# Kernel tuning notes

Measured on AMD Instinct MI355X. Metric: run time of the kernel, lower is better.

The kernel has to match this reference:

```python
import jax, jax.numpy as jnp
import numpy as np

B, S, D = 2, 2048, 1024
H, DK, DV = 16, 64, 64
D_OUT = 1024


def setup_inputs() -> dict:
    key = jax.random.key(0)
    ks = jax.random.split(key, 9)
    sd = 1.0 / np.sqrt(D)
    # Linear weights stored as [in, out] (torch applies x @ W.T with W [out,in])
    return {
        "x": jax.random.normal(ks[0], (B, S, D), dtype=jnp.float32),
        "Wq": jax.random.normal(ks[1], (D, H * DK), dtype=jnp.float32) * sd,
        "bq": jnp.zeros((H * DK,), dtype=jnp.float32),
        "Wk": jax.random.normal(ks[2], (D, H * DK), dtype=jnp.float32) * sd,
        "bk": jnp.zeros((H * DK,), dtype=jnp.float32),
        "Wv": jax.random.normal(ks[3], (D, H * DV), dtype=jnp.float32) * sd,
        "bv": jnp.zeros((H * DV,), dtype=jnp.float32),
        "Wo": jax.random.normal(ks[4], (H * DV, D_OUT), dtype=jnp.float32) * sd,
        "bo": jnp.zeros((D_OUT,), dtype=jnp.float32),
    }


def _attn(x, Wq, bq, Wk, bk, Wv, bv, Wo, bo):
    n = x.shape[-2]
    q = (x @ Wq + bq).reshape(B, n, H, DK).transpose(0, 2, 1, 3)  # [B,H,S,DK]
    k = (x @ Wk + bk).reshape(B, n, H, DK).transpose(0, 2, 1, 3)
    v = (x @ Wv + bv).reshape(B, n, H, DV).transpose(0, 2, 1, 3)
    scores = jnp.einsum("bhqd,bhkd->bhqk", q / jnp.sqrt(jnp.float32(DK)), k)
    # causal additive mask: 0 on/below diagonal, -inf above (matches 1 - 1/tril)
    causal = jnp.tril(jnp.ones((n, n), dtype=bool))
    scores = jnp.where(causal, scores, -jnp.inf)
    probs = jax.nn.softmax(scores, axis=-1)
    out = jnp.einsum("bhqk,bhkd->bhqd", probs, v)  # [B,H,S,DV]
    out = out.transpose(0, 2, 1, 3).reshape(B, n, H * DV)
    return out @ Wo + bo


def reference(x, Wq, bq, Wk, bk, Wv, bv, Wo, bo):
    return _attn(x, Wq, bq, Wk, bk, Wv, bv, Wo, bo)
```

## Files before the change

### kernel.cpp

```cpp
#include <hip/hip_runtime.h>

typedef unsigned short u16;
typedef __bf16 bf16_t;
typedef bf16_t bf16x8 __attribute__((ext_vector_type(8)));
typedef float f32x4 __attribute__((ext_vector_type(4)));

#define DEV __device__ __forceinline__
#define LOG2E 1.4426950408889634f
#define QKS (0.125f * LOG2E)

static_assert(sizeof(bf16x8) == 16, "bf16x8 must be 16B");

DEV u16 f2b(float v) { return __builtin_bit_cast(u16, (bf16_t)v); }
DEV float b2f(u16 v) { return (float)__builtin_bit_cast(bf16_t, v); }

DEV void g2l16(const void* g, void* l) {
  __builtin_amdgcn_global_load_lds(
      (const __attribute__((address_space(1))) void*)g,
      (__attribute__((address_space(3))) void*)l, 16, 0, 0);
}

DEV int sniff_is_f32(const u16* __restrict__ W) {
  const int lane = threadIdx.x & 63;
  int cnt = 0;
#pragma unroll
  for (int i = 0; i < 8; i++) {
    u16 u = W[(lane * 8 + i) * 2];
    cnt += (((u >> 7) & 0xFF) >= 126) ? 1 : 0;
  }
#pragma unroll
  for (int off = 1; off < 64; off <<= 1) cnt += __shfl_xor(cnt, off, 64);
  return cnt > 128;
}


__global__ __launch_bounds__(256) void convert_x_k(
    const void* __restrict__ xin, const u16* __restrict__ Wsniff,
    u16* __restrict__ xb) {
  const int i = (blockIdx.x * 256 + threadIdx.x) * 8;
  if (sniff_is_f32(Wsniff)) {
    const float* xf = (const float*)xin;
    float4 a = *(const float4*)&xf[i];
    float4 b = *(const float4*)&xf[i + 4];
    u16 o[8] = {f2b(a.x), f2b(a.y), f2b(a.z), f2b(a.w),
                f2b(b.x), f2b(b.y), f2b(b.z), f2b(b.w)};
    *(uint4*)&xb[i] = *(const uint4*)o;
  } else {
    *(uint4*)&xb[i] = *(const uint4*)((const u16*)xin + i);
  }
}

__global__ __launch_bounds__(256) void transpose_k(
    const void* __restrict__ Wq, const void* __restrict__ Wk,
    const void* __restrict__ Wv, const void* __restrict__ Wo,
    const void* __restrict__ bq, const void* __restrict__ bk,
    const void* __restrict__ bv, const void* __restrict__ bo,
    u16* __restrict__ Wqkv_t, u16* __restrict__ Wo_t,
    u16* __restrict__ bqkv_b, u16* __restrict__ bo_b) {
  __shared__ u16 tile[64][68];
  const int z = blockIdx.z;
  const void* src = (z == 0) ? Wq : (z == 1) ? Wk : (z == 2) ? Wv : Wo;
  u16* dst = (z < 3) ? (Wqkv_t + (size_t)z * 1024 * 1024) : Wo_t;
  const int k0 = blockIdx.y * 64, n0 = blockIdx.x * 64;
  const int t = threadIdx.x;
  const int r = t >> 4, c4 = (t & 15) * 4;
  const int isf = sniff_is_f32((const u16*)Wq);

  if (blockIdx.x == 0 && blockIdx.y == 0) {
    const void* bsrc = (z == 0) ? bq : (z == 1) ? bk : (z == 2) ? bv : bo;
    u16* bdst = (z < 3) ? (bqkv_b + z * 1024) : bo_b;
#pragma unroll
    for (int i = 0; i < 4; i++) {
      const int idx = t + i * 256;
      const float v =
          isf ? ((const float*)bsrc)[idx] : b2f(((const u16*)bsrc)[idx]);
      bdst[idx] = f2b(v);
    }
  }

#pragma unroll
  for (int i = 0; i < 4; i++) {
    int rr = r + i * 16;
    const size_t base = (size_t)(k0 + rr) * 1024 + n0 + c4;
    if (isf) {
      float4 v = *(const float4*)((const float*)src + base);
      tile[rr][c4] = f2b(v.x); tile[rr][c4 + 1] = f2b(v.y);
      tile[rr][c4 + 2] = f2b(v.z); tile[rr][c4 + 3] = f2b(v.w);
    } else {
      ushort4 v = *(const ushort4*)((const u16*)src + base);
      tile[rr][c4] = v.x; tile[rr][c4 + 1] = v.y;
      tile[rr][c4 + 2] = v.z; tile[rr][c4 + 3] = v.w;
    }
  }
  __syncthreads();
#pragma unroll
  for (int i = 0; i < 4; i++) {
    int rr = r + i * 16;
    ushort4 v;
    v.x = tile[c4][rr]; v.y = tile[c4 + 1][rr];
    v.z = tile[c4 + 2][rr]; v.w = tile[c4 + 3][rr];
    *(ushort4*)&dst[(size_t)(n0 + rr) * 1024 + k0 + c4] = v;
  }
}

template <int MODE>
__global__ __launch_bounds__(256, 3) void gemm_k(
    const u16* __restrict__ A, const u16* __restrict__ Bt,
    const u16* __restrict__ bias, void* __restrict__ o0v,
    u16* __restrict__ o1, u16* __restrict__ o2,
    const u16* __restrict__ Wsniff, int M, int N, int K) {
  alignas(16) __shared__ u16 smem[2][128][64];
  u16(*As)[64] = smem[0];
  u16(*Bs)[64] = smem[1];
  const int tid = threadIdx.x;
  const int wave = tid >> 6, lane = tid & 63;
  const int quad = lane >> 4, l16 = lane & 15;
  const int m0 = blockIdx.y * 128, n0 = blockIdx.x * 128;
  const int wr = (wave >> 1) * 64, wc = (wave & 1) * 64;
  const int sw = l16 & 7;

  f32x4 acc[4][4];
#pragma unroll
  for (int i = 0; i < 4; i++)
#pragma unroll
    for (int j = 0; j < 4; j++) acc[i][j] = (f32x4){0.f, 0.f, 0.f, 0.f};

  const int srow = lane >> 3, schunk = lane & 7;
  const int cs = schunk ^ srow;

  for (int k0 = 0; k0 < K; k0 += 64) {
    __syncthreads();
#pragma unroll
    for (int j = 0; j < 8; j++) {
      const int t = wave * 8 + j;
      if (t < 16) {
        const int row = t * 8 + srow;
        g2l16(&A[(size_t)(m0 + row) * K + k0 + cs * 8], &As[t * 8][0]);
      } else {
        const int t2 = t - 16;
        const int row = t2 * 8 + srow;
        g2l16(&Bt[(size_t)(n0 + row) * K + k0 + cs * 8], &Bs[t2 * 8][0]);
      }
    }
    __syncthreads();
#pragma unroll
    for (int kk = 0; kk < 2; kk++) {
      const int pos = ((kk << 2) | quad) ^ sw;
      bf16x8 af[4], bfr[4];
#pragma unroll
      for (int mi = 0; mi < 4; mi++)
        af[mi] = *(const bf16x8*)&As[wr + mi * 16 + l16][pos * 8];
#pragma unroll
      for (int ni = 0; ni < 4; ni++)
        bfr[ni] = *(const bf16x8*)&Bs[wc + ni * 16 + l16][pos * 8];
#pragma unroll
      for (int mi = 0; mi < 4; mi++)
#pragma unroll
        for (int ni = 0; ni < 4; ni++)
          acc[mi][ni] = __builtin_amdgcn_mfma_f32_16x16x32_bf16(
              af[mi], bfr[ni], acc[mi][ni], 0, 0, 0);
    }
  }

  if (MODE == 0 && n0 >= 2048) {
    u16* T = &smem[0][0][0];
    const int b = m0 >> 11, sb = m0 & 2047;
#pragma unroll
    for (int r2 = 0; r2 < 2; r2++) {
      __syncthreads();
      if (wc == r2 * 64) {
#pragma unroll
        for (int mi = 0; mi < 4; mi++)
#pragma unroll
          for (int ni = 0; ni < 4; ni++) {
            const int c = ni * 16 + l16;
            const int col = n0 + r2 * 64 + c;
            const float bv_ = b2f(bias[col]);
#pragma unroll
            for (int r = 0; r < 4; r++) {
              const int s = wr + mi * 16 + quad * 4 + r;
              T[c * 136 + s] = f2b(acc[mi][ni][r] + bv_);
            }
          }
      }
      __syncthreads();
      {
        const int c = tid >> 2, s8 = (tid & 3) * 32;
        const int nn = (n0 - 2048) + r2 * 64 + c;
        const int h = nn >> 6, d = nn & 63;
        u16* dst = &o2[(((size_t)(b * 16 + h) * 64) + d) * 2048 + sb];
#pragma unroll
        for (int j2 = 0; j2 < 4; j2++)
          *(uint4*)&dst[s8 + j2 * 8] = *(const uint4*)&T[c * 136 + s8 + j2 * 8];
      }
    }
    return;
  }

  const int isf = (MODE == 1) ? sniff_is_f32(Wsniff) : 0;
#pragma unroll
  for (int mi = 0; mi < 4; mi++) {
    const int rbase = m0 + wr + mi * 16 + quad * 4;
#pragma unroll
    for (int ni = 0; ni < 4; ni++) {
      const int col = n0 + wc + ni * 16 + l16;
      const float bv_ = b2f(bias[col]);
      if (MODE == 0) {
        const int seg = col >> 10;
        const int nn = col & 1023;
        const int h = nn >> 6, d = nn & 63;
        u16* op = (seg == 0) ? (u16*)o0v : o1;
#pragma unroll
        for (int r = 0; r < 4; r++) {
          const int m = rbase + r;
          const int b = m >> 11, s = m & 2047;
          float v = acc[mi][ni][r] + bv_;
          if (seg == 0) v *= QKS;
          op[(((size_t)(b * 16 + h) * 2048) + s) * 64 + d] = f2b(v);
        }
      } else {
#pragma unroll
        for (int r = 0; r < 4; r++) {
          const int m = rbase + r;
          const float v = acc[mi][ni][r] + bv_;
          if (isf) ((float*)o0v)[(size_t)m * N + col] = v;
          else     ((u16*)o0v)[(size_t)m * N + col] = f2b(v);
        }
      }
    }
  }
}

__global__ __launch_bounds__(512, 4) void attn_k(
    const u16* __restrict__ Q, const u16* __restrict__ K,
    const u16* __restrict__ Vt, u16* __restrict__ p0, u16* __restrict__ p1,
    float* __restrict__ l0, float* __restrict__ l1) {
  alignas(16) __shared__ u16 Ks[2][128][64];
  alignas(16) __shared__ u16 Vs[2][64][128];
  alignas(16) __shared__ u16 PsT[128][64];
  const int tid = threadIdx.x;
  const int w = tid >> 6, lane = tid & 63;
  const int quad = lane >> 4, l16 = lane & 15;
  const int split = blockIdx.x & 1;
  const int pairIdx = blockIdx.x >> 1;
  const int bh = blockIdx.y;
  const int b = bh >> 4, h = bh & 15;
  const int sw = l16 & 7;

  u16* Op = split ? p1 : p0;
  float* lp = split ? l1 : l0;

  const int krow_off = lane >> 3, kchunk = lane & 7;
  const int vrow_off = lane >> 4, vchunk = lane & 15;

  for (int pi = 0; pi < 2; pi++) {
    const int qt = pi ? (15 - pairIdx) : pairIdx;
    const int q0 = qt * 128;
    const int wrow = q0 + w * 16;
    const int nkt = qt + 1;
    const int cnt = (nkt - split + 1) >> 1;

    bf16x8 aq[2];
#pragma unroll
    for (int kc = 0; kc < 2; kc++)
      aq[kc] = *(const bf16x8*)&Q[((size_t)bh * 2048 + wrow + l16) * 64 +
                                  kc * 32 + quad * 8];

    f32x4 oacc[4];
#pragma unroll
    for (int di = 0; di < 4; di++) oacc[di] = (f32x4){0.f, 0.f, 0.f, 0.f};
    float lrp = 0.f;

    auto stage = [&](int buf, int kts) {
      const int k0s = kts * 128;
#pragma unroll
      for (int j = 0; j < 4; j++) {
        const int t = w * 4 + j;
        if (t < 16) {
          const int r = t * 8 + krow_off;
          const int cs = kchunk ^ (r & 7);
          g2l16(&K[((size_t)bh * 2048 + k0s + r) * 64 + cs * 8],
                &Ks[buf][t * 8][0]);
        } else {
          const int t2 = t - 16;
          const int r = t2 * 4 + vrow_off;
          const int cs = vchunk ^ (r & 7);
          g2l16(&Vt[((size_t)bh * 64 + r) * 2048 + k0s + cs * 8],
                &Vs[buf][t2 * 4][0]);
        }
      }
    };

    if (cnt > 0) stage(0, split);
    for (int ti = 0; ti < cnt; ti++) {
      const int cur = ti & 1;
      const int k0 = (split + 2 * ti) * 128;
      if (ti + 1 < cnt) {
        stage(cur ^ 1, split + 2 * (ti + 1));
        asm volatile("s_waitcnt vmcnt(4)" ::: "memory");
      } else {
        asm volatile("s_waitcnt vmcnt(0)" ::: "memory");
      }
      asm volatile("s_barrier" ::: "memory");

#pragma unroll
      for (int h2 = 0; h2 < 2; h2++) {
        const int k0h = k0 + h2 * 64;
        if (k0h > wrow + 15) continue;
        const bool needmask = (k0h + 63 > wrow);

        f32x4 st[4];
#pragma unroll
        for (int nk = 0; nk < 4; nk++) st[nk] = (f32x4){0.f, 0.f, 0.f, 0.f};
#pragma unroll
        for (int kc = 0; kc < 2; kc++)
#pragma unroll
          for (int nk = 0; nk < 4; nk++) {
            const int pos = ((kc << 2) | quad) ^ sw;
            bf16x8 kf =
                *(const bf16x8*)&Ks[cur][h2 * 64 + nk * 16 + l16][pos * 8];
            st[nk] = __builtin_amdgcn_mfma_f32_16x16x32_bf16(kf, aq[kc],
                                                             st[nk], 0, 0, 0);
          }

        const int q_glob = wrow + l16;
#pragma unroll
        for (int nk = 0; nk < 4; nk++) {
          const int kbase = k0h + nk * 16 + quad * 4;
          u16 pk[4];
#pragma unroll
          for (int r = 0; r < 4; r++) {
            float p = __builtin_amdgcn_exp2f(st[nk][r]);
            if (needmask && (kbase + r > q_glob)) p = 0.f;
            lrp += p;
            pk[r] = f2b(p);
          }
          const int g = nk * 4 + quad;
          const int cc = (g >> 1) ^ sw;
          *(uint2*)&PsT[w * 16 + l16][cc * 8 + (g & 1) * 4] =
              *(const uint2*)pk;
        }
        asm volatile("s_waitcnt lgkmcnt(0)" ::: "memory");

#pragma unroll
        for (int kc = 0; kc < 2; kc++) {
          const int pcc = ((kc << 2) | quad) ^ sw;
          bf16x8 ap = *(const bf16x8*)&PsT[w * 16 + l16][pcc * 8];
#pragma unroll
          for (int di = 0; di < 4; di++) {
            const int pos = ((h2 << 3) | (kc << 2) | quad) ^ sw;
            bf16x8 vf = *(const bf16x8*)&Vs[cur][di * 16 + l16][pos * 8];
            oacc[di] = __builtin_amdgcn_mfma_f32_16x16x32_bf16(
                ap, vf, oacc[di], 0, 0, 0);
          }
        }
      }
      asm volatile("s_barrier" ::: "memory");
    }

    lrp += __shfl_xor(lrp, 16, 64);
    lrp += __shfl_xor(lrp, 32, 64);
    if (lane < 16) lp[(size_t)bh * 2048 + wrow + lane] = lrp;

#pragma unroll
    for (int di = 0; di < 4; di++)
#pragma unroll
      for (int r = 0; r < 4; r++) {
        const int row = wrow + quad * 4 + r;
        Op[((size_t)b * 2048 + row) * 1024 + h * 64 + di * 16 + l16] =
            f2b(oacc[di][r]);
      }
  }
}

__global__ __launch_bounds__(256) void norm_k(
    const u16* __restrict__ p0, const u16* __restrict__ p1,
    const float* __restrict__ l0, const float* __restrict__ l1,
    u16* __restrict__ out) {
  const int i = (blockIdx.x * 256 + threadIdx.x) * 8;
  const int row = i >> 10;
  const int col = i & 1023;
  const int bh = ((row >> 11) << 4) | (col >> 6);
  const int q = row & 2047;
  const size_t li = (size_t)bh * 2048 + q;
  const float rc = 1.0f / (l0[li] + l1[li]);
  uint4 a = *(const uint4*)&p0[i];
  uint4 bb = *(const uint4*)&p1[i];
  const u16* au = (const u16*)&a;
  const u16* bu = (const u16*)&bb;
  u16 o[8];
#pragma unroll
  for (int j = 0; j < 8; j++) o[j] = f2b((b2f(au[j]) + b2f(bu[j])) * rc);
  *(uint4*)&out[i] = *(const uint4*)o;
}

extern "C" void kernel_launch(void* const* d_in, const int* in_sizes, int n_in,
                              void* d_out, int out_size, void* d_ws,
                              size_t ws_size, hipStream_t stream) {
  const void* x  = d_in[0];
  const void* Wq = d_in[1];
  const void* bq = d_in[2];
  const void* Wk = d_in[3];
  const void* bk = d_in[4];
  const void* Wv = d_in[5];
  const void* bv = d_in[6];
  const void* Wo = d_in[7];
  const void* bo = d_in[8];

  char* ws = (char*)d_ws;
  u16* xb     = (u16*)ws;          ws += (size_t)4096 * 1024 * 2;
  u16* Wqkv_t = (u16*)ws;          ws += (size_t)3072 * 1024 * 2;
  u16* Wo_t   = (u16*)ws;          ws += (size_t)1024 * 1024 * 2;
  u16* bqkv_b = (u16*)ws;          ws += 3072 * 2;
  u16* bo_b   = (u16*)ws;          ws += 1024 * 2 + 128;
  u16* Qb     = (u16*)ws;          ws += (size_t)4096 * 1024 * 2;
  u16* Kb     = (u16*)ws;          ws += (size_t)4096 * 1024 * 2;
  u16* Vtb    = (u16*)ws;          ws += (size_t)4096 * 1024 * 2;
  u16* p1     = (u16*)ws;          ws += (size_t)4096 * 1024 * 2;
  float* l0   = (float*)ws;        ws += (size_t)32 * 2048 * 4;
  float* l1   = (float*)ws;        ws += (size_t)32 * 2048 * 4;
  u16* p0     = xb;
  u16* Ob     = xb;

  convert_x_k<<<2048, 256, 0, stream>>>(x, (const u16*)Wq, xb);
  transpose_k<<<dim3(16, 16, 4), 256, 0, stream>>>(Wq, Wk, Wv, Wo, bq, bk, bv,
                                                   bo, Wqkv_t, Wo_t, bqkv_b,
                                                   bo_b);
  gemm_k<0><<<dim3(24, 32), 256, 0, stream>>>(xb, Wqkv_t, bqkv_b, Qb, Kb, Vtb,
                                              (const u16*)Wq, 4096, 3072, 1024);
  attn_k<<<dim3(16, 32), 512, 0, stream>>>(Qb, Kb, Vtb, p0, p1, l0, l1);
  norm_k<<<2048, 256, 0, stream>>>(p0, p1, l0, l1, Ob);
  gemm_k<1><<<dim3(8, 32), 256, 0, stream>>>(Ob, Wo_t, bo_b, d_out, nullptr,
                                             nullptr, (const u16*)Wq, 4096,
                                             1024, 1024);
}
```

Before: 199.2 us.

## Merge x conversion into weight prep kernel and pipeline both attention query tiles

Folds the x fp32-to-bf16 conversion into the weight transpose kernel as an extra grid slice, removing one kernel launch. In the attention kernel, the two query tiles each block handles are processed in one continuous K/V tile loop instead of two separate loops. This lets the double-buffered prefetch of the second tile's first K/V block overlap the first tile's last compute, so the pipeline no longer drains and refills between tiles. It keeps Q fragments for both tiles in registers, which raises register pressure, and adds a mid-loop epilogue plus accumulator reset.

```diff
diff --git a/kernel.cpp b/kernel.cpp
--- a/kernel.cpp
+++ b/kernel.cpp
@@ -34,37 +34,43 @@
 }
 
 
-__global__ __launch_bounds__(256) void convert_x_k(
-    const void* __restrict__ xin, const u16* __restrict__ Wsniff,
-    u16* __restrict__ xb) {
-  const int i = (blockIdx.x * 256 + threadIdx.x) * 8;
-  if (sniff_is_f32(Wsniff)) {
-    const float* xf = (const float*)xin;
-    float4 a = *(const float4*)&xf[i];
-    float4 b = *(const float4*)&xf[i + 4];
-    u16 o[8] = {f2b(a.x), f2b(a.y), f2b(a.z), f2b(a.w),
-                f2b(b.x), f2b(b.y), f2b(b.z), f2b(b.w)};
-    *(uint4*)&xb[i] = *(const uint4*)o;
-  } else {
-    *(uint4*)&xb[i] = *(const uint4*)((const u16*)xin + i);
-  }
-}
-
-__global__ __launch_bounds__(256) void transpose_k(
+__global__ __launch_bounds__(256) void prep_k(
     const void* __restrict__ Wq, const void* __restrict__ Wk,
     const void* __restrict__ Wv, const void* __restrict__ Wo,
     const void* __restrict__ bq, const void* __restrict__ bk,
     const void* __restrict__ bv, const void* __restrict__ bo,
-    u16* __restrict__ Wqkv_t, u16* __restrict__ Wo_t,
-    u16* __restrict__ bqkv_b, u16* __restrict__ bo_b) {
+    const void* __restrict__ xin, u16* __restrict__ Wqkv_t,
+    u16* __restrict__ Wo_t, u16* __restrict__ bqkv_b, u16* __restrict__ bo_b,
+    u16* __restrict__ xb) {
   __shared__ u16 tile[64][68];
   const int z = blockIdx.z;
+  const int t = threadIdx.x;
+  const int isf = sniff_is_f32((const u16*)Wq);
+
+  if (z == 4) {
+    const int bi = blockIdx.y * 16 + blockIdx.x;
+    const int base = bi * 16384 + t * 8;
+#pragma unroll
+    for (int it = 0; it < 8; it++) {
+      const int i = base + it * 2048;
+      if (isf) {
+        const float* xf = (const float*)xin;
+        float4 a = *(const float4*)&xf[i];
+        float4 b = *(const float4*)&xf[i + 4];
+        u16 o[8] = {f2b(a.x), f2b(a.y), f2b(a.z), f2b(a.w),
+                    f2b(b.x), f2b(b.y), f2b(b.z), f2b(b.w)};
+        *(uint4*)&xb[i] = *(const uint4*)o;
+      } else {
+        *(uint4*)&xb[i] = *(const uint4*)((const u16*)xin + i);
+      }
+    }
+    return;
+  }
+
   const void* src = (z == 0) ? Wq : (z == 1) ? Wk : (z == 2) ? Wv : Wo;
   u16* dst = (z < 3) ? (Wqkv_t + (size_t)z * 1024 * 1024) : Wo_t;
   const int k0 = blockIdx.y * 64, n0 = blockIdx.x * 64;
-  const int t = threadIdx.x;
   const int r = t >> 4, c4 = (t & 15) * 4;
-  const int isf = sniff_is_f32((const u16*)Wq);
 
   if (blockIdx.x == 0 && blockIdx.y == 0) {
     const void* bsrc = (z == 0) ? bq : (z == 1) ? bk : (z == 2) ? bv : bo;
@@ -253,115 +259,55 @@
   const int krow_off = lane >> 3, kchunk = lane & 7;
   const int vrow_off = lane >> 4, vchunk = lane & 15;
 
-  for (int pi = 0; pi < 2; pi++) {
-    const int qt = pi ? (15 - pairIdx) : pairIdx;
-    const int q0 = qt * 128;
-    const int wrow = q0 + w * 16;
-    const int nkt = qt + 1;
-    const int cnt = (nkt - split + 1) >> 1;
-
-    bf16x8 aq[2];
+  const int qtA = pairIdx, qtB = 15 - pairIdx;
+  const int cntA = (qtA + 2 - split) >> 1;
+  const int cntB = (qtB + 2 - split) >> 1;
+  const int tot = cntA + cntB;
+  const int wrowP[2] = {qtA * 128 + w * 16, qtB * 128 + w * 16};
+
+  bf16x8 aq[2][2];
+#pragma unroll
+  for (int pi = 0; pi < 2; pi++)
 #pragma unroll
     for (int kc = 0; kc < 2; kc++)
-      aq[kc] = *(const bf16x8*)&Q[((size_t)bh * 2048 + wrow + l16) * 64 +
-                                  kc * 32 + quad * 8];
-
-    f32x4 oacc[4];
-#pragma unroll
-    for (int di = 0; di < 4; di++) oacc[di] = (f32x4){0.f, 0.f, 0.f, 0.f};
-    float lrp = 0.f;
-
-    auto stage = [&](int buf, int kts) {
-      const int k0s = kts * 128;
-#pragma unroll
-      for (int j = 0; j < 4; j++) {
-        const int t = w * 4 + j;
-        if (t < 16) {
-          const int r = t * 8 + krow_off;
-          const int cs = kchunk ^ (r & 7);
-          g2l16(&K[((size_t)bh * 2048 + k0s + r) * 64 + cs * 8],
-                &Ks[buf][t * 8][0]);
-        } else {
-          const int t2 = t - 16;
-          const int r = t2 * 4 + vrow_off;
-          const int cs = vchunk ^ (r & 7);
-          g2l16(&Vt[((size_t)bh * 64 + r) * 2048 + k0s + cs * 8],
-                &Vs[buf][t2 * 4][0]);
-        }
-      }
-    };
-
-    if (cnt > 0) stage(0, split);
-    for (int ti = 0; ti < cnt; ti++) {
-      const int cur = ti & 1;
-      const int k0 = (split + 2 * ti) * 128;
-      if (ti + 1 < cnt) {
-        stage(cur ^ 1, split + 2 * (ti + 1));
-        asm volatile("s_waitcnt vmcnt(4)" ::: "memory");
+      aq[pi][kc] = *(const bf16x8*)&Q[((size_t)bh * 2048 + wrowP[pi] + l16) *
+                                          64 + kc * 32 + quad * 8];
+
+  f32x4 oacc[4];
+#pragma unroll
+  for (int di = 0; di < 4; di++) oacc[di] = (f32x4){0.f, 0.f, 0.f, 0.f};
+  float lrp = 0.f;
+
+  auto tileK0 = [&](int idx) {
+    const int ti = (idx >= cntA) ? idx - cntA : idx;
+    return (split + 2 * ti) * 128;
+  };
+
+  auto stage = [&](int buf, int k0s) {
+#pragma unroll
+    for (int j = 0; j < 4; j++) {
+      const int t = w * 4 + j;
+      if (t < 16) {
+        const int r = t * 8 + krow_off;
+        const int cs = kchunk ^ (r & 7);
+        g2l16(&K[((size_t)bh * 2048 + k0s + r) * 64 + cs * 8],
+              &Ks[buf][t * 8][0]);
       } else {
-        asm volatile("s_waitcnt vmcnt(0)" ::: "memory");
-      }
-      asm volatile("s_barrier" ::: "memory");
-
-#pragma unroll
-      for (int h2 = 0; h2 < 2; h2++) {
-        const int k0h = k0 + h2 * 64;
-        if (k0h > wrow + 15) continue;
-        const bool needmask = (k0h + 63 > wrow);
-
-        f32x4 st[4];
-#pragma unroll
-        for (int nk = 0; nk < 4; nk++) st[nk] = (f32x4){0.f, 0.f, 0.f, 0.f};
-#pragma unroll
-        for (int kc = 0; kc < 2; kc++)
-#pragma unroll
-          for (int nk = 0; nk < 4; nk++) {
-            const int pos = ((kc << 2) | quad) ^ sw;
-            bf16x8 kf =
-                *(const bf16x8*)&Ks[cur][h2 * 64 + nk * 16 + l16][pos * 8];
-            st[nk] = __builtin_amdgcn_mfma_f32_16x16x32_bf16(kf, aq[kc],
-                                                             st[nk], 0, 0, 0);
-          }
-
-        const int q_glob = wrow + l16;
-#pragma unroll
-        for (int nk = 0; nk < 4; nk++) {
-          const int kbase = k0h + nk * 16 + quad * 4;
-          u16 pk[4];
-#pragma unroll
-          for (int r = 0; r < 4; r++) {
-            float p = __builtin_amdgcn_exp2f(st[nk][r]);
-            if (needmask && (kbase + r > q_glob)) p = 0.f;
-            lrp += p;
-            pk[r] = f2b(p);
-          }
-          const int g = nk * 4 + quad;
-          const int cc = (g >> 1) ^ sw;
-          *(uint2*)&PsT[w * 16 + l16][cc * 8 + (g & 1) * 4] =
-              *(const uint2*)pk;
-        }
-        asm volatile("s_waitcnt lgkmcnt(0)" ::: "memory");
-
-#pragma unroll
-        for (int kc = 0; kc < 2; kc++) {
-          const int pcc = ((kc << 2) | quad) ^ sw;
-          bf16x8 ap = *(const bf16x8*)&PsT[w * 16 + l16][pcc * 8];
-#pragma unroll
-          for (int di = 0; di < 4; di++) {
-            const int pos = ((h2 << 3) | (kc << 2) | quad) ^ sw;
-            bf16x8 vf = *(const bf16x8*)&Vs[cur][di * 16 + l16][pos * 8];
-            oacc[di] = __builtin_amdgcn_mfma_f32_16x16x32_bf16(
-                ap, vf, oacc[di], 0, 0, 0);
-          }
-        }
-      }
-      asm volatile("s_barrier" ::: "memory");
-    }
-
-    lrp += __shfl_xor(lrp, 16, 64);
-    lrp += __shfl_xor(lrp, 32, 64);
-    if (lane < 16) lp[(size_t)bh * 2048 + wrow + lane] = lrp;
-
+        const int t2 = t - 16;
+        const int r = t2 * 4 + vrow_off;
+        const int cs = vchunk ^ (r & 7);
+        g2l16(&Vt[((size_t)bh * 64 + r) * 2048 + k0s + cs * 8],
+              &Vs[buf][t2 * 4][0]);
+      }
+    }
+  };
+
+  auto epilogue = [&](int pi) {
+    const int wrow = wrowP[pi];
+    float s = lrp;
+    s += __shfl_xor(s, 16, 64);
+    s += __shfl_xor(s, 32, 64);
+    if (lane < 16) lp[(size_t)bh * 2048 + wrow + lane] = s;
 #pragma unroll
     for (int di = 0; di < 4; di++)
 #pragma unroll
@@ -370,7 +316,86 @@
         Op[((size_t)b * 2048 + row) * 1024 + h * 64 + di * 16 + l16] =
             f2b(oacc[di][r]);
       }
-  }
+  };
+
+  if (cntA == 0) epilogue(0);
+
+  stage(0, tileK0(0));
+  for (int idx = 0; idx < tot; idx++) {
+    const int cur = idx & 1;
+    const int pi = (idx >= cntA) ? 1 : 0;
+    const int k0 = tileK0(idx);
+    const int wrow = wrowP[pi];
+    if (idx + 1 < tot) {
+      stage(cur ^ 1, tileK0(idx + 1));
+      asm volatile("s_waitcnt vmcnt(4)" ::: "memory");
+    } else {
+      asm volatile("s_waitcnt vmcnt(0)" ::: "memory");
+    }
+    asm volatile("s_barrier" ::: "memory");
+
+#pragma unroll
+    for (int h2 = 0; h2 < 2; h2++) {
+      const int k0h = k0 + h2 * 64;
+      if (k0h > wrow + 15) continue;
+      const bool needmask = (k0h + 63 > wrow);
+
+      f32x4 st[4];
+#pragma unroll
+      for (int nk = 0; nk < 4; nk++) st[nk] = (f32x4){0.f, 0.f, 0.f, 0.f};
+#pragma unroll
+      for (int kc = 0; kc < 2; kc++)
+#pragma unroll
+        for (int nk = 0; nk < 4; nk++) {
+          const int pos = ((kc << 2) | quad) ^ sw;
+          bf16x8 kf =
+              *(const bf16x8*)&Ks[cur][h2 * 64 + nk * 16 + l16][pos * 8];
+          st[nk] = __builtin_amdgcn_mfma_f32_16x16x32_bf16(kf, aq[pi][kc],
+                                                           st[nk], 0, 0, 0);
+        }
+
+      const int q_glob = wrow + l16;
+#pragma unroll
+      for (int nk = 0; nk < 4; nk++) {
+        const int kbase = k0h + nk * 16 + quad * 4;
+        u16 pk[4];
+#pragma unroll
+        for (int r = 0; r < 4; r++) {
+          float p = __builtin_amdgcn_exp2f(st[nk][r]);
+          if (needmask && (kbase + r > q_glob)) p = 0.f;
+          lrp += p;
+          pk[r] = f2b(p);
+        }
+        const int g = nk * 4 + quad;
+        const int cc = (g >> 1) ^ sw;
+        *(uint2*)&PsT[w * 16 + l16][cc * 8 + (g & 1) * 4] = *(const uint2*)pk;
+      }
+      asm volatile("s_waitcnt lgkmcnt(0)" ::: "memory");
+
+#pragma unroll
+      for (int kc = 0; kc < 2; kc++) {
+        const int pcc = ((kc << 2) | quad) ^ sw;
+        bf16x8 ap = *(const bf16x8*)&PsT[w * 16 + l16][pcc * 8];
+#pragma unroll
+        for (int di = 0; di < 4; di++) {
+          const int pos = ((h2 << 3) | (kc << 2) | quad) ^ sw;
+          bf16x8 vf = *(const bf16x8*)&Vs[cur][di * 16 + l16][pos * 8];
+          oacc[di] = __builtin_amdgcn_mfma_f32_16x16x32_bf16(ap, vf, oacc[di],
+                                                             0, 0, 0);
+        }
+      }
+    }
+
+    if (idx == cntA - 1) {
+      epilogue(0);
+      lrp = 0.f;
+#pragma unroll
+      for (int di = 0; di < 4; di++) oacc[di] = (f32x4){0.f, 0.f, 0.f, 0.f};
+    }
+    asm volatile("s_barrier" ::: "memory");
+  }
+
+  epilogue(1);
 }
 
 __global__ __launch_bounds__(256) void norm_k(
@@ -422,10 +447,9 @@
   u16* p0     = xb;
   u16* Ob     = xb;
 
-  convert_x_k<<<2048, 256, 0, stream>>>(x, (const u16*)Wq, xb);
-  transpose_k<<<dim3(16, 16, 4), 256, 0, stream>>>(Wq, Wk, Wv, Wo, bq, bk, bv,
-                                                   bo, Wqkv_t, Wo_t, bqkv_b,
-                                                   bo_b);
+  prep_k<<<dim3(16, 16, 5), 256, 0, stream>>>(Wq, Wk, Wv, Wo, bq, bk, bv, bo,
+                                              x, Wqkv_t, Wo_t, bqkv_b, bo_b,
+                                              xb);
   gemm_k<0><<<dim3(24, 32), 256, 0, stream>>>(xb, Wqkv_t, bqkv_b, Qb, Kb, Vtb,
                                               (const u16*)Wq, 4096, 3072, 1024);
   attn_k<<<dim3(16, 32), 512, 0, stream>>>(Qb, Kb, Vtb, p0, p1, l0, l1);
```

After: 198.2 us. About the same (-0.5%).
